# Kernel tuning notes

Hardware: AMD Instinct MI355X
Metric: run time of the kernel (lower is better)

The kernel has to match this reference:

```python
import jax, jax.numpy as jnp
import numpy as np

D_MODEL = 512
MAX_LEN = 4096
B, P, Q = 32, 2048, 2048
VOCABS = (7, 24, 288)


def _make_pe(max_len, d):
    # pe[pos, 2k] = sin(pos / 10000**(2k/d)), pe[pos, 2k+1] = cos(same angle)
    pos = jnp.arange(max_len, dtype=jnp.float32)[:, None]
    i = jnp.arange(0, d, 2, dtype=jnp.float32)
    ang = pos / jnp.power(10000.0, i / d)          # [max_len, d/2]
    pe = jnp.stack([jnp.sin(ang), jnp.cos(ang)], axis=-1).reshape(max_len, d)
    return pe


def setup_inputs() -> dict:
    key = jax.random.key(0)
    ks = jax.random.split(key, 12)
    inp = {}
    names = ["in0", "tg0", "in1", "tg1", "in2", "tg2"]
    vocabs = [7, 7, 24, 24, 288, 288]
    for n, v, k in zip(names, vocabs, ks[:6]):
        inp[n] = jax.random.randint(k, (B, P), 0, v, dtype=jnp.int64 if jax.config.jax_enable_x64 else jnp.int32)
    inp["emb0"] = jax.random.normal(ks[6], (VOCABS[0], D_MODEL), jnp.float32) * 0.02
    inp["emb1"] = jax.random.normal(ks[7], (VOCABS[1], D_MODEL), jnp.float32) * 0.02
    inp["emb2"] = jax.random.normal(ks[8], (VOCABS[2], D_MODEL), jnp.float32) * 0.02
    inp["pe"] = _make_pe(MAX_LEN, D_MODEL)
    fan_in = (len(VOCABS) + 1) * D_MODEL
    bound = 1.0 / np.sqrt(fan_in)
    inp["W"] = jax.random.uniform(ks[9], (fan_in, D_MODEL), jnp.float32, -bound, bound)
    inp["b"] = jax.random.uniform(ks[10], (D_MODEL,), jnp.float32, -bound, bound)
    return inp


def reference(in0, tg0, in1, tg1, in2, tg2, emb0, emb1, emb2, pe, W, b):
    def encode(i0, i1, i2):
        Bk, L = i0.shape
        pos = jnp.broadcast_to(pe[:L], (Bk, L, pe.shape[1]))
        feats = jnp.concatenate([emb0[i0], emb1[i1], emb2[i2], pos], axis=-1)  # [B, L, 4*d]
        return feats @ W + b                                                   # [B, L, d]

    return encode(in0, in1, in2), encode(tg0, tg1, tg2)
```

## Files before the change

kernel.cpp:

```cpp
#include <hip/hip_runtime.h>


#define TM 32
#define TN 64
#define TK 16
#define KSPLIT 4
#define TROWS 2367

typedef float vfloat4 __attribute__((ext_vector_type(4)));

__global__ __launch_bounds__(256) void te_gemm_partial(
    const float* __restrict__ emb0, const float* __restrict__ emb1,
    const float* __restrict__ emb2, const float* __restrict__ pe,
    const float* __restrict__ W, float* __restrict__ P)
{
    __shared__ float As[TK][TM + 4];
    __shared__ float Bs[TK][TN + 4];

    const int nt  = blockIdx.x;
    const int mt  = blockIdx.y;
    const int kz  = blockIdx.z;
    const int tid = threadIdx.x;

    const float* A; int M; int m0; int wrow; int tbase;
    if (mt == 0)       { A = emb0; M = 7;    m0 = 0;            wrow = 0;    tbase = 0;   }
    else if (mt == 1)  { A = emb1; M = 24;   m0 = 0;            wrow = 512;  tbase = 7;   }
    else if (mt < 11)  { A = emb2; M = 288;  m0 = (mt-2)*TM;    wrow = 1024; tbase = 31;  }
    else               { A = pe;   M = 2048; m0 = (mt-11)*TM;   wrow = 1536; tbase = 319; }

    const int n0 = nt * TN;
    const int kbase = kz * 128;

    const int ar = tid >> 2;
    const int ac = (tid & 3) * 4;
    const int br = tid >> 4;
    const int bc = (tid & 15) * 4;

    const int my = (tid >> 4) * 2;
    const int mx = (tid & 15) * 4;

    float acc[2][4];
    #pragma unroll
    for (int i = 0; i < 2; i++)
        #pragma unroll
        for (int j = 0; j < 4; j++) acc[i][j] = 0.f;

    for (int k0 = 0; k0 < 128; k0 += TK) {
        float4 av = make_float4(0.f, 0.f, 0.f, 0.f);
        if (ar < TM && (m0 + ar) < M)
            av = *(const float4*)&A[(size_t)(m0 + ar) * 512 + kbase + k0 + ac];
        float4 bv = *(const float4*)&W[(size_t)(wrow + kbase + k0 + br) * 512 + n0 + bc];

        __syncthreads();
        if (ar < TM) {
            As[ac + 0][ar] = av.x;
            As[ac + 1][ar] = av.y;
            As[ac + 2][ar] = av.z;
            As[ac + 3][ar] = av.w;
        }
        *(float4*)&Bs[br][bc] = bv;
        __syncthreads();

        #pragma unroll
        for (int k = 0; k < TK; k++) {
            float2 a2 = *(const float2*)&As[k][my];
            float4 b4 = *(const float4*)&Bs[k][mx];
            acc[0][0] += a2.x * b4.x; acc[0][1] += a2.x * b4.y;
            acc[0][2] += a2.x * b4.z; acc[0][3] += a2.x * b4.w;
            acc[1][0] += a2.y * b4.x; acc[1][1] += a2.y * b4.y;
            acc[1][2] += a2.y * b4.z; acc[1][3] += a2.y * b4.w;
        }
    }

    #pragma unroll
    for (int i = 0; i < 2; i++) {
        int row = m0 + my + i;
        if (row < M) {
            *(float4*)&P[((size_t)kz * TROWS + tbase + row) * 512 + n0 + mx] =
                make_float4(acc[i][0], acc[i][1], acc[i][2], acc[i][3]);
        }
    }
}

__global__ __launch_bounds__(256) void te_reduce(
    const float* __restrict__ P, const float* __restrict__ bias,
    float* __restrict__ T)
{
    const int idx4 = blockIdx.x * 256 + threadIdx.x;
    if (idx4 >= TROWS * 128) return;
    const int row = idx4 >> 7;
    const int d4  = idx4 & 127;

    const float4* P4 = (const float4*)P;
    const size_t stride4 = (size_t)TROWS * 128;
    float4 s = P4[idx4];
    #pragma unroll
    for (int kz = 1; kz < KSPLIT; kz++) {
        float4 v = P4[kz * stride4 + idx4];
        s.x += v.x; s.y += v.y; s.z += v.z; s.w += v.w;
    }
    if (row >= 319) {
        float4 bb = ((const float4*)bias)[d4];
        s.x += bb.x; s.y += bb.y; s.z += bb.z; s.w += bb.w;
    }
    ((float4*)T)[idx4] = s;
}

__global__ __launch_bounds__(256) void te_gather_add(
    const int* __restrict__ in0, const int* __restrict__ tg0,
    const int* __restrict__ in1, const int* __restrict__ tg1,
    const int* __restrict__ in2, const int* __restrict__ tg2,
    const float* __restrict__ T, float* __restrict__ out)
{
    const int gid = blockIdx.x * 256 + threadIdx.x;
    const int d4  = gid & 127;
    const int row = gid >> 7;
    const int l   = row & 2047;
    const int bl  = row & 65535;
    const int o   = row >> 16;

    const int* __restrict__ p0 = o ? tg0 : in0;
    const int* __restrict__ p1 = o ? tg1 : in1;
    const int* __restrict__ p2 = o ? tg2 : in2;
    const int i0 = p0[bl];
    const int i1 = p1[bl];
    const int i2 = p2[bl];

    const float4* __restrict__ T0 = (const float4*)T;
    const float4* __restrict__ T1 = (const float4*)(T + 7 * 512);
    const float4* __restrict__ T2 = (const float4*)(T + 31 * 512);
    const float4* __restrict__ Tp = (const float4*)(T + 319 * 512);

    const float4 a = T0[i0 * 128 + d4];
    const float4 b = T1[i1 * 128 + d4];
    const float4 c = T2[i2 * 128 + d4];
    const float4 p = Tp[l  * 128 + d4];

    vfloat4 r;
    r.x = a.x + b.x + c.x + p.x;
    r.y = a.y + b.y + c.y + p.y;
    r.z = a.z + b.z + c.z + p.z;
    r.w = a.w + b.w + c.w + p.w;

    __builtin_nontemporal_store(r, ((vfloat4*)out) + gid);
}

extern "C" void kernel_launch(void* const* d_in, const int* in_sizes, int n_in,
                              void* d_out, int out_size, void* d_ws, size_t ws_size,
                              hipStream_t stream) {
    const int*   in0  = (const int*)  d_in[0];
    const int*   tg0  = (const int*)  d_in[1];
    const int*   in1  = (const int*)  d_in[2];
    const int*   tg1  = (const int*)  d_in[3];
    const int*   in2  = (const int*)  d_in[4];
    const int*   tg2  = (const int*)  d_in[5];
    const float* emb0 = (const float*)d_in[6];
    const float* emb1 = (const float*)d_in[7];
    const float* emb2 = (const float*)d_in[8];
    const float* pe   = (const float*)d_in[9];
    const float* W    = (const float*)d_in[10];
    const float* bias = (const float*)d_in[11];
    float* out = (float*)d_out;
    float* T   = (float*)d_ws;
    float* P   = T + (size_t)TROWS * 512;

    dim3 ggrid(8, 75, KSPLIT);
    te_gemm_partial<<<ggrid, 256, 0, stream>>>(emb0, emb1, emb2, pe, W, P);

    te_reduce<<<(TROWS * 128 + 255) / 256, 256, 0, stream>>>(P, bias, T);

    te_gather_add<<<65536, 256, 0, stream>>>(in0, tg0, in1, tg1, in2, tg2, T, out);
}
```

Before: 360.0 us.

## Precombine emb0/emb1 projections into pair table and reuse PE row across batch

The reduce kernel now builds a combined 7x24 table holding the summed projected emb0 and emb1 rows, so the gather kernel loads three vectors per output element instead of four. The gather kernel is reorganized so each block handles one sequence position for all 32 batch rows. It loads the positional row once, stages the indices in shared memory, and loops over the batch. This cuts gather loads and index arithmetic in a kernel dominated by output writes, at the cost of strided index loads and fewer blocks.

```diff
diff --git a/kernel.cpp b/kernel.cpp
--- a/kernel.cpp
+++ b/kernel.cpp
@@ -5,7 +5,8 @@
 #define TN 64
 #define TK 16
 #define KSPLIT 4
-#define TROWS 2367
+#define PROWS 2367
+#define TROWS 2504
 
 typedef float vfloat4 __attribute__((ext_vector_type(4)));
 
@@ -76,7 +77,7 @@
     for (int i = 0; i < 2; i++) {
         int row = m0 + my + i;
         if (row < M) {
-            *(float4*)&P[((size_t)kz * TROWS + tbase + row) * 512 + n0 + mx] =
+            *(float4*)&P[((size_t)kz * PROWS + tbase + row) * 512 + n0 + mx] =
                 make_float4(acc[i][0], acc[i][1], acc[i][2], acc[i][3]);
         }
     }
@@ -92,16 +93,36 @@
     const int d4  = idx4 & 127;
 
     const float4* P4 = (const float4*)P;
-    const size_t stride4 = (size_t)TROWS * 128;
-    float4 s = P4[idx4];
-    #pragma unroll
-    for (int kz = 1; kz < KSPLIT; kz++) {
-        float4 v = P4[kz * stride4 + idx4];
+    const size_t stride4 = (size_t)PROWS * 128;
+
+    float4 s;
+    if (row < 168) {
+        const int i0 = row / 24;
+        const int i1 = row - i0 * 24;
+        const int r0 = i0 * 128 + d4;
+        const int r1 = (7 + i1) * 128 + d4;
+        s = P4[r0];
+        float4 v = P4[r1];
         s.x += v.x; s.y += v.y; s.z += v.z; s.w += v.w;
-    }
-    if (row >= 319) {
-        float4 bb = ((const float4*)bias)[d4];
-        s.x += bb.x; s.y += bb.y; s.z += bb.z; s.w += bb.w;
+        #pragma unroll
+        for (int kz = 1; kz < KSPLIT; kz++) {
+            float4 a = P4[kz * stride4 + r0];
+            float4 b = P4[kz * stride4 + r1];
+            s.x += a.x + b.x; s.y += a.y + b.y;
+            s.z += a.z + b.z; s.w += a.w + b.w;
+        }
+    } else {
+        const int ri = (row - 137) * 128 + d4;
+        s = P4[ri];
+        #pragma unroll
+        for (int kz = 1; kz < KSPLIT; kz++) {
+            float4 v = P4[kz * stride4 + ri];
+            s.x += v.x; s.y += v.y; s.z += v.z; s.w += v.w;
+        }
+        if (row >= 456) {
+            float4 bb = ((const float4*)bias)[d4];
+            s.x += bb.x; s.y += bb.y; s.z += bb.z; s.w += bb.w;
+        }
     }
     ((float4*)T)[idx4] = s;
 }
@@ -112,37 +133,49 @@
     const int* __restrict__ in2, const int* __restrict__ tg2,
     const float* __restrict__ T, float* __restrict__ out)
 {
-    const int gid = blockIdx.x * 256 + threadIdx.x;
-    const int d4  = gid & 127;
-    const int row = gid >> 7;
-    const int l   = row & 2047;
-    const int bl  = row & 65535;
-    const int o   = row >> 16;
-
-    const int* __restrict__ p0 = o ? tg0 : in0;
-    const int* __restrict__ p1 = o ? tg1 : in1;
-    const int* __restrict__ p2 = o ? tg2 : in2;
-    const int i0 = p0[bl];
-    const int i1 = p1[bl];
-    const int i2 = p2[bl];
-
-    const float4* __restrict__ T0 = (const float4*)T;
-    const float4* __restrict__ T1 = (const float4*)(T + 7 * 512);
-    const float4* __restrict__ T2 = (const float4*)(T + 31 * 512);
-    const float4* __restrict__ Tp = (const float4*)(T + 319 * 512);
-
-    const float4 a = T0[i0 * 128 + d4];
-    const float4 b = T1[i1 * 128 + d4];
-    const float4 c = T2[i2 * 128 + d4];
-    const float4 p = Tp[l  * 128 + d4];
-
-    vfloat4 r;
-    r.x = a.x + b.x + c.x + p.x;
-    r.y = a.y + b.y + c.y + p.y;
-    r.z = a.z + b.z + c.z + p.z;
-    r.w = a.w + b.w + c.w + p.w;
-
-    __builtin_nontemporal_store(r, ((vfloat4*)out) + gid);
+    __shared__ int s_i01[32];
+    __shared__ int s_i2[32];
+
+    const int bid = blockIdx.x;
+    const int o   = bid >> 11;
+    const int l   = bid & 2047;
+    const int tid = threadIdx.x;
+
+    if (tid < 32) {
+        const int* __restrict__ p0 = o ? tg0 : in0;
+        const int* __restrict__ p1 = o ? tg1 : in1;
+        const int* __restrict__ p2 = o ? tg2 : in2;
+        const int i0 = p0[tid * 2048 + l];
+        const int i1 = p1[tid * 2048 + l];
+        s_i01[tid] = i0 * 24 + i1;
+        s_i2[tid]  = p2[tid * 2048 + l];
+    }
+    __syncthreads();
+
+    const int d4 = tid & 127;
+    const int bo = tid >> 7;
+
+    const float4* __restrict__ T01 = (const float4*)T;
+    const float4* __restrict__ T2  = (const float4*)(T + 168 * 512);
+    const float4* __restrict__ Tp  = (const float4*)(T + 456 * 512);
+
+    const float4 p = Tp[l * 128 + d4];
+
+    vfloat4* __restrict__ obase =
+        (vfloat4*)out + ((size_t)o * 32 * 2048 + l) * 128 + d4;
+
+    #pragma unroll 4
+    for (int bi = 0; bi < 16; bi++) {
+        const int b = bi * 2 + bo;
+        const float4 a = T01[s_i01[b] * 128 + d4];
+        const float4 c = T2 [s_i2 [b] * 128 + d4];
+        vfloat4 r;
+        r.x = a.x + c.x + p.x;
+        r.y = a.y + c.y + p.y;
+        r.z = a.z + c.z + p.z;
+        r.w = a.w + c.w + p.w;
+        __builtin_nontemporal_store(r, obase + (size_t)b * 2048 * 128);
+    }
 }
 
 extern "C" void kernel_launch(void* const* d_in, const int* in_sizes, int n_in,
@@ -169,5 +202,5 @@
 
     te_reduce<<<(TROWS * 128 + 255) / 256, 256, 0, stream>>>(P, bias, T);
 
-    te_gather_add<<<65536, 256, 0, stream>>>(in0, tg0, in1, tg1, in2, tg2, T, out);
-}
+    te_gather_add<<<4096, 256, 0, stream>>>(in0, tg0, in1, tg1, in2, tg2, T, out);
+}
```

New measurement: 336.7 us. -6.5%, faster.
